# Kernel tuning notes

Hardware: AMD Instinct MI355X
Metric: run time of the kernel (lower is better)

Reference implementation:

```python
import jax, jax.numpy as jnp
import numpy as np

# Mamba-2 dims (from wrapper: d_model=hidden_size=2048, d_state=64, d_conv=4, expand=2, headdim=64)
D_MODEL = 2048
EXPAND = 2
HEADDIM = 64
D_STATE = 64
D_CONV = 4
D_INNER = EXPAND * D_MODEL            # 4096
NHEADS = D_INNER // HEADDIM           # 64
NGROUPS = 1                           # mamba_ssm default
CONV_DIM = D_INNER + 2 * NGROUPS * D_STATE          # 4224
D_IN_PROJ = 2 * D_INNER + 2 * NGROUPS * D_STATE + NHEADS  # 8384
BATCH = 1
SEQLEN = 1024
RMS_EPS = 1e-5


def setup_inputs() -> dict:
    key = jax.random.key(0)
    ks = jax.random.split(key, 8)
    x = jax.random.normal(ks[0], (BATCH, SEQLEN, D_MODEL), jnp.float32)
    W_in = jax.random.normal(ks[1], (D_IN_PROJ, D_MODEL), jnp.float32) * 0.02
    conv_w = jax.random.normal(ks[2], (CONV_DIM, D_CONV), jnp.float32) * 0.2
    conv_b = jnp.zeros((CONV_DIM,), jnp.float32)
    # dt_bias so that softplus(dt_raw + dt_bias) lands in a realistic dt range ~[1e-3, 5e-2]
    dt_bias = jax.random.uniform(ks[3], (NHEADS,), jnp.float32, -6.0, -3.0)
    # A = -exp(A_log), A_log init like mamba_ssm: A ~ Uniform(1, 16)
    A_log = jnp.log(1.0 + 15.0 * jax.random.uniform(ks[4], (NHEADS,), jnp.float32))
    D = jnp.ones((NHEADS,), jnp.float32)
    norm_w = jnp.ones((D_INNER,), jnp.float32)
    W_out = jax.random.normal(ks[5], (D_MODEL, D_INNER), jnp.float32) * 0.02
    return {"x": x, "W_in": W_in, "conv_w": conv_w, "conv_b": conv_b,
            "dt_bias": dt_bias, "A_log": A_log, "D": D, "norm_w": norm_w, "W_out": W_out}


def reference(x, W_in, conv_w, conv_b, dt_bias, A_log, D, norm_w, W_out):
    B, T, _ = x.shape
    # input projection -> [z | xBC | dt]
    zxbcdt = jnp.einsum('btd,pd->btp', x, W_in)
    z = zxbcdt[..., :D_INNER]                                  # [B,T,D_INNER] gate
    xBC = zxbcdt[..., D_INNER:D_INNER + CONV_DIM]              # [B,T,CONV_DIM]
    dt = jax.nn.softplus(zxbcdt[..., D_INNER + CONV_DIM:] + dt_bias)  # [B,T,H]
    # causal depthwise conv1d (kernel D_CONV) + SiLU
    xp = jnp.pad(xBC, ((0, 0), (D_CONV - 1, 0), (0, 0)))
    conv = conv_b + sum(xp[:, k:k + T, :] * conv_w[:, k] for k in range(D_CONV))
    xBC = jax.nn.silu(conv)
    xh = xBC[..., :D_INNER].reshape(B, T, NHEADS, HEADDIM)     # [B,T,H,P]
    Bm = xBC[..., D_INNER:D_INNER + D_STATE]                   # [B,T,N] (ngroups=1)
    Cm = xBC[..., D_INNER + D_STATE:]                          # [B,T,N]
    A = -jnp.exp(A_log)                                        # [H], negative
    dA = jnp.exp(dt * A)                                       # [B,T,H] decay per step

    def step(h, inp):
        # h: [B,H,P,N]
        dA_t, dt_t, B_t, x_t, C_t = inp
        h = h * dA_t[:, :, None, None] + jnp.einsum('bh,bn,bhp->bhpn', dt_t, B_t, x_t)
        y_t = jnp.einsum('bhpn,bn->bhp', h, C_t)
        return h, y_t

    h0 = jnp.zeros((B, NHEADS, HEADDIM, D_STATE), x.dtype)
    xs = (dA.transpose(1, 0, 2), dt.transpose(1, 0, 2), Bm.transpose(1, 0, 2),
          xh.transpose(1, 0, 2, 3), Cm.transpose(1, 0, 2))
    _, ys = jax.lax.scan(step, h0, xs)                         # ys: [T,B,H,P]
    y = ys.transpose(1, 0, 2, 3) + D[None, None, :, None] * xh  # skip term D*x
    y = y.reshape(B, T, D_INNER)
    # gated RMSNorm (norm_before_gate=False): norm(y * silu(z)) * weight
    y = y * jax.nn.silu(z)
    y = y * jax.lax.rsqrt(jnp.mean(y * y, axis=-1, keepdims=True) + RMS_EPS) * norm_w
    return jnp.einsum('bti,di->btd', y, W_out)
```

## Files before the change

### kernel.cpp

```cpp
#include <hip/hip_runtime.h>
#include <hip/hip_bf16.h>
#include <stdint.h>

#define SEQLEN   1024
#define DMODEL   2048
#define DINNER   4096
#define NHEADS   64
#define HEADDIM  64
#define DSTATE   64
#define CONVDIM  4224
#define DINPROJ  8384
#define RMS_EPS  1e-5f
#define CPAD     68
#define LP       72

typedef __attribute__((ext_vector_type(8))) __bf16 bf16x8;
typedef __attribute__((ext_vector_type(8))) unsigned short us8;
typedef __attribute__((ext_vector_type(4))) float f32x4;

__device__ __forceinline__ ushort f2bf(float f) {
    uint32_t u = __float_as_uint(f);
    u += 0x7FFFu + ((u >> 16) & 1u);
    return (ushort)(u >> 16);
}

__device__ __forceinline__ float bf2f(ushort u) {
    return __uint_as_float((uint32_t)u << 16);
}

__device__ __forceinline__ float silu(float a) { return a / (1.f + __expf(-a)); }

__device__ __forceinline__ void gload_lds16(const void* g, void* l) {
    __builtin_amdgcn_global_load_lds(
        (const __attribute__((address_space(1))) void*)g,
        (__attribute__((address_space(3))) void*)l, 16, 0, 0);
}

__global__ __launch_bounds__(256) void cvt3_kernel(
    const float* __restrict__ a, ushort* __restrict__ oa, int na4,
    const float* __restrict__ b, ushort* __restrict__ ob, int nb4,
    const float* __restrict__ c, ushort* __restrict__ oc, int nc4)
{
    int i = blockIdx.x * 256 + threadIdx.x;
    const float* src; ushort* dst;
    if (i < na4) { src = a; dst = oa; }
    else if (i < na4 + nb4) { i -= na4; src = b; dst = ob; }
    else { i -= na4 + nb4; if (i >= nc4) return; src = c; dst = oc; }
    float4 v = ((const float4*)src)[i];
    ushort4 o;
    o.x = f2bf(v.x); o.y = f2bf(v.y); o.z = f2bf(v.z); o.w = f2bf(v.w);
    ((ushort4*)dst)[i] = o;
}

__global__ __launch_bounds__(256, 4) void gemm4_bf16_nt(
    const __bf16* __restrict__ A, const __bf16* __restrict__ B,
    float* __restrict__ C, int M, int N, int K,
    int ntx, int nty, int nk, int ksteps, int swz)
{
    __shared__ __align__(16) __bf16 As[2][128 * 32];
    __shared__ __align__(16) __bf16 Bs[2][128 * 32];
    const int tid  = threadIdx.x;
    const int lane = tid & 63;
    const int wave = tid >> 6;
    const int wr = wave >> 1, wc = wave & 1;
    int id = blockIdx.x;
    if (swz) { int q = (ntx * nty * nk) >> 3; id = (id & 7) * q + (id >> 3); }
    const int kz  = id / (ntx * nty);
    const int rem = id % (ntx * nty);
    const int tx = rem / nty, ty = rem % nty;
    const int row0 = ty * 128, col0 = tx * 128;
    const int lr = lane & 15, lq = lane >> 4;
    const int rA = lane >> 2, jl = lane & 3;
    const int k0 = kz * ksteps * 32;

    const __bf16* srcA[2];
    const __bf16* srcB[2];
    int dstAB[2];
    #pragma unroll
    for (int e = 0; e < 2; ++e) {
        int r0 = (wave * 2 + e) * 16;
        int r  = r0 + rA;
        int jg = jl ^ ((rA >> 1) & 3);
        srcA[e] = A + (size_t)(row0 + r) * K + k0 + jg * 8;
        int gb = col0 + r; if (gb > N - 1) gb = N - 1;
        srcB[e] = B + (size_t)gb * K + k0 + jg * 8;
        dstAB[e] = r0 * 32;
    }

    f32x4 acc[4][4] = {};
    const int nt = ksteps;

#define STAGE(BUF)                                                            \
    _Pragma("unroll")                                                         \
    for (int e = 0; e < 2; ++e) {                                             \
        gload_lds16(srcA[e], &As[BUF][dstAB[e]]);                             \
        gload_lds16(srcB[e], &Bs[BUF][dstAB[e]]);                             \
        srcA[e] += 32; srcB[e] += 32;                                         \
    }

#define COMPUTE(BUF)                                                          \
    {                                                                         \
        bf16x8 af[4], bfr[4];                                                 \
        const int sl = (lq ^ ((lr >> 1) & 3)) * 8;                            \
        _Pragma("unroll")                                                     \
        for (int m = 0; m < 4; ++m) {                                         \
            int r = wr * 64 + m * 16 + lr;                                    \
            af[m] = *(const bf16x8*)(&As[BUF][r * 32 + sl]);                  \
        }                                                                     \
        _Pragma("unroll")                                                     \
        for (int n = 0; n < 4; ++n) {                                         \
            int r = wc * 64 + n * 16 + lr;                                    \
            bfr[n] = *(const bf16x8*)(&Bs[BUF][r * 32 + sl]);                 \
        }                                                                     \
        __builtin_amdgcn_s_setprio(1);                                        \
        _Pragma("unroll")                                                     \
        for (int m = 0; m < 4; ++m)                                           \
            _Pragma("unroll")                                                 \
            for (int n = 0; n < 4; ++n)                                       \
                acc[m][n] = __builtin_amdgcn_mfma_f32_16x16x32_bf16(af[m], bfr[n], acc[m][n], 0, 0, 0); \
        __builtin_amdgcn_s_setprio(0);                                        \
    }

    STAGE(0);
    asm volatile("s_waitcnt vmcnt(0)" ::: "memory");
    __builtin_amdgcn_s_barrier();
    asm volatile("" ::: "memory");

    for (int t = 0; t < nt; t += 2) {
        STAGE(1);
        COMPUTE(0);
        asm volatile("s_waitcnt vmcnt(0)" ::: "memory");
        __builtin_amdgcn_s_barrier();
        asm volatile("" ::: "memory");
        if (t + 2 < nt) { STAGE(0); }
        COMPUTE(1);
        asm volatile("s_waitcnt vmcnt(0)" ::: "memory");
        __builtin_amdgcn_s_barrier();
        asm volatile("" ::: "memory");
    }
#undef STAGE
#undef COMPUTE

    float* Co = C + (size_t)kz * M * N;
    #pragma unroll
    for (int m = 0; m < 4; ++m)
        #pragma unroll
        for (int n = 0; n < 4; ++n) {
            int col = col0 + wc * 64 + n * 16 + lr;
            if (col < N) {
                #pragma unroll
                for (int j = 0; j < 4; ++j) {
                    int row = row0 + wr * 64 + m * 16 + lq * 4 + j;
                    Co[(size_t)row * N + col] = acc[m][n][j];
                }
            }
        }
}

__global__ __launch_bounds__(256) void reduce4_scale_kernel(
    const float* __restrict__ p, const float* __restrict__ ssbuf,
    float* __restrict__ out, int n4)
{
    int i = blockIdx.x * 256 + threadIdx.x;
    if (i < n4) {
        int t = i >> 9;
        float sc = rsqrtf(ssbuf[t] * (1.f / DINNER) + RMS_EPS);
        float4 a = ((const float4*)p)[i];
        float4 b = ((const float4*)p)[i + n4];
        float4 c = ((const float4*)p)[i + 2 * (size_t)n4];
        float4 d = ((const float4*)p)[i + 3 * (size_t)n4];
        float4 o = {(a.x + b.x + c.x + d.x) * sc, (a.y + b.y + c.y + d.y) * sc,
                    (a.z + b.z + c.z + d.z) * sc, (a.w + b.w + c.w + d.w) * sc};
        ((float4*)out)[i] = o;
    }
}

__global__ __launch_bounds__(256, 4) void chunk_intra_kernel(
    const float* __restrict__ zx, const float* __restrict__ conv_w,
    const float* __restrict__ conv_b, const float* __restrict__ dt_bias,
    const float* __restrict__ A_log,
    float* __restrict__ x_scan, float* __restrict__ Cb,
    float* __restrict__ yintra, float* __restrict__ Tc, float* __restrict__ Ssum)
{
    const int head  = blockIdx.x >> 4;
    const int chunk = blockIdx.x & 15;
    const int t0 = chunk * 64;
    const int tid = threadIdx.x;
    const int lane = tid & 63, wv = tid >> 6;
    const int lr = lane & 15, lq = lane >> 4;

    __shared__ __align__(16) ushort XT [64 * LP];
    __shared__ __align__(16) ushort Crm[64 * LP];
    __shared__ __align__(16) ushort Brm[64 * LP];
    __shared__ __align__(16) ushort BnT[64 * LP];
    __shared__ float Sc[64], dts[64], ws[64];

    {
        const int p = lane;
        const int c = head * 64 + p;
        const float w0 = conv_w[c*4+0], w1 = conv_w[c*4+1];
        const float w2 = conv_w[c*4+2], w3 = conv_w[c*4+3];
        const float bia = conv_b[c];
        const int gt0 = t0 + wv * 16;
        const float* zc = zx + DINNER + c;
        float xm3 = (gt0 >= 3) ? zc[(size_t)(gt0-3)*DINPROJ] : 0.f;
        float xm2 = (gt0 >= 2) ? zc[(size_t)(gt0-2)*DINPROJ] : 0.f;
        float xm1 = (gt0 >= 1) ? zc[(size_t)(gt0-1)*DINPROJ] : 0.f;
        uint32_t pk[8];
        #pragma unroll
        for (int e = 0; e < 16; ++e) {
            float xt = zc[(size_t)(gt0+e)*DINPROJ];
            float s  = silu(bia + xm3*w0 + xm2*w1 + xm1*w2 + xt*w3);
            x_scan[(size_t)(gt0+e)*DINNER + c] = s;
            ushort b = f2bf(s);
            if (e & 1) pk[e>>1] |= (uint32_t)b << 16; else pk[e>>1] = (uint32_t)b;
            xm3 = xm2; xm2 = xm1; xm1 = xt;
        }
        int4 lo = { (int)pk[0], (int)pk[1], (int)pk[2], (int)pk[3] };
        int4 hi = { (int)pk[4], (int)pk[5], (int)pk[6], (int)pk[7] };
        *(int4*)&XT[p * LP + wv*16]     = lo;
        *(int4*)&XT[p * LP + wv*16 + 8] = hi;
    }

    #pragma unroll
    for (int k = 0; k < 4; ++k) {
        int n0 = wv * 16 + k * 4;
        int gt = t0 + lane;
        {
            float4 w0 = *(const float4*)&conv_w[(4096 + n0 + 0) * 4];
            float4 w1 = *(const float4*)&conv_w[(4096 + n0 + 1) * 4];
            float4 w2 = *(const float4*)&conv_w[(4096 + n0 + 2) * 4];
            float4 w3 = *(const float4*)&conv_w[(4096 + n0 + 3) * 4];
            float4 bv = *(const float4*)&conv_b[4096 + n0];
            float4 r0 = {0,0,0,0}, r1 = {0,0,0,0}, r2 = {0,0,0,0}, r3;
            const float* base = zx + (size_t)gt * DINPROJ + 8192 + n0;
            if (gt >= 3) r0 = *(const float4*)(base - 3 * DINPROJ);
            if (gt >= 2) r1 = *(const float4*)(base - 2 * DINPROJ);
            if (gt >= 1) r2 = *(const float4*)(base - 1 * DINPROJ);
            r3 = *(const float4*)base;
            ushort b0 = f2bf(silu(bv.x + r0.x*w0.x + r1.x*w0.y + r2.x*w0.z + r3.x*w0.w));
            ushort b1 = f2bf(silu(bv.y + r0.y*w1.x + r1.y*w1.y + r2.y*w1.z + r3.y*w1.w));
            ushort b2 = f2bf(silu(bv.z + r0.z*w2.x + r1.z*w2.y + r2.z*w2.z + r3.z*w2.w));
            ushort b3 = f2bf(silu(bv.w + r0.w*w3.x + r1.w*w3.y + r2.w*w3.z + r3.w*w3.w));
            uint2 pk = { (uint32_t)b0 | ((uint32_t)b1 << 16),
                         (uint32_t)b2 | ((uint32_t)b3 << 16) };
            *(uint2*)&Brm[lane * LP + n0] = pk;
            BnT[(n0+0)*LP + lane] = b0; BnT[(n0+1)*LP + lane] = b1;
            BnT[(n0+2)*LP + lane] = b2; BnT[(n0+3)*LP + lane] = b3;
        }
        {
            float4 w0 = *(const float4*)&conv_w[(4160 + n0 + 0) * 4];
            float4 w1 = *(const float4*)&conv_w[(4160 + n0 + 1) * 4];
            float4 w2 = *(const float4*)&conv_w[(4160 + n0 + 2) * 4];
            float4 w3 = *(const float4*)&conv_w[(4160 + n0 + 3) * 4];
            float4 bv = *(const float4*)&conv_b[4160 + n0];
            float4 r0 = {0,0,0,0}, r1 = {0,0,0,0}, r2 = {0,0,0,0}, r3;
            const float* base = zx + (size_t)gt * DINPROJ + 8256 + n0;
            if (gt >= 3) r0 = *(const float4*)(base - 3 * DINPROJ);
            if (gt >= 2) r1 = *(const float4*)(base - 2 * DINPROJ);
            if (gt >= 1) r2 = *(const float4*)(base - 1 * DINPROJ);
            r3 = *(const float4*)base;
            float4 cv;
            cv.x = silu(bv.x + r0.x*w0.x + r1.x*w0.y + r2.x*w0.z + r3.x*w0.w);
            cv.y = silu(bv.y + r0.y*w1.x + r1.y*w1.y + r2.y*w1.z + r3.y*w1.w);
            cv.z = silu(bv.z + r0.z*w2.x + r1.z*w2.y + r2.z*w2.z + r3.z*w2.w);
            cv.w = silu(bv.w + r0.w*w3.x + r1.w*w3.y + r2.w*w3.z + r3.w*w3.w);
            uint2 pk = { (uint32_t)f2bf(cv.x) | ((uint32_t)f2bf(cv.y) << 16),
                         (uint32_t)f2bf(cv.z) | ((uint32_t)f2bf(cv.w) << 16) };
            *(uint2*)&Crm[lane * LP + n0] = pk;
            if (head == 0) *(float4*)&Cb[(size_t)gt * 64 + n0] = cv;
        }
    }

    if (wv == 1) {
        float raw = zx[(size_t)(t0 + lane) * DINPROJ + 8320 + head] + dt_bias[head];
        float dt  = (raw > 20.f) ? raw : log1pf(__expf(raw));
        dts[lane] = dt;
        float v = dt * (-__expf(A_log[head]));
        #pragma unroll
        for (int off = 1; off < 64; off <<= 1) {
            float u = __shfl_up(v, off, 64);
            if (lane >= off) v += u;
        }
        Sc[lane] = v;
        Ssum[(t0 + lane) * 64 + head] = v;
    }
    __syncthreads();
    if (tid < 64) ws[tid] = dts[tid] * __expf(Sc[63] - Sc[tid]);

    const int i0 = wv * 16;
    f32x4 gf[4] = {};
    #pragma unroll
    for (int kk = 0; kk < 2; ++kk) {
        bf16x8 a = __builtin_bit_cast(bf16x8,
            *(const us8*)&Crm[(i0 + lr) * LP + lq*8 + kk*32]);
        #pragma unroll
        for (int f = 0; f < 4; ++f) {
            bf16x8 b = __builtin_bit_cast(bf16x8,
                *(const us8*)&Brm[(f*16 + lr) * LP + lq*8 + kk*32]);
            gf[f] = __builtin_amdgcn_mfma_f32_16x16x32_bf16(a, b, gf[f], 0, 0, 0);
        }
    }
    {
        float Si[4];
        #pragma unroll
        for (int j = 0; j < 4; ++j) Si[j] = Sc[i0 + lq*4 + j];
        #pragma unroll
        for (int f = 0; f < 4; ++f) {
            int s = f*16 + lr;
            float dw = dts[s], Ss_ = Sc[s];
            #pragma unroll
            for (int j = 0; j < 4; ++j) {
                int i = i0 + lq*4 + j;
                float v = (s <= i) ? gf[f][j] * dw * __expf(Si[j] - Ss_) : 0.f;
                Crm[i * LP + s] = f2bf(v);
            }
        }
    }
    __syncthreads();

    const int p0 = i0;
    bf16x8 xa[2], xw[2];
    #pragma unroll
    for (int kk = 0; kk < 2; ++kk) {
        us8 raw = *(const us8*)&XT[(p0 + lr) * LP + lq*8 + kk*32];
        xa[kk] = __builtin_bit_cast(bf16x8, raw);
        us8 sw;
        #pragma unroll
        for (int e = 0; e < 8; ++e) {
            int s = lq*8 + kk*32 + e;
            sw[e] = f2bf(bf2f(raw[e]) * ws[s]);
        }
        xw[kk] = __builtin_bit_cast(bf16x8, sw);
    }
    f32x4 yf[4] = {};
    f32x4 tf[4] = {};
    #pragma unroll
    for (int kk = 0; kk < 2; ++kk) {
        #pragma unroll
        for (int f = 0; f < 4; ++f) {
            bf16x8 gb = __builtin_bit_cast(bf16x8,
                *(const us8*)&Crm[(f*16 + lr) * LP + lq*8 + kk*32]);
            yf[f] = __builtin_amdgcn_mfma_f32_16x16x32_bf16(xa[kk], gb, yf[f], 0, 0, 0);
            bf16x8 bb = __builtin_bit_cast(bf16x8,
                *(const us8*)&BnT[(f*16 + lr) * LP + lq*8 + kk*32]);
            tf[f] = __builtin_amdgcn_mfma_f32_16x16x32_bf16(xw[kk], bb, tf[f], 0, 0, 0);
        }
    }
    float* tcb = Tc + (size_t)(head * 16 + chunk) * 4096;
    #pragma unroll
    for (int f = 0; f < 4; ++f) {
        int col = f*16 + lr;
        int p   = p0 + lq*4;
        float4 yv = {yf[f][0], yf[f][1], yf[f][2], yf[f][3]};
        *(float4*)&yintra[(size_t)(t0 + col) * DINNER + head*64 + p] = yv;
        #pragma unroll
        for (int j = 0; j < 4; ++j)
            tcb[(p + j) * 64 + col] = tf[f][j];
    }
}

__global__ __launch_bounds__(256) void chunk_state_kernel(
    float* __restrict__ Tc, const float* __restrict__ Ssum)
{
    const int head = blockIdx.x;
    const int tid = threadIdx.x;
    float h[16] = {};
    float* base = Tc + (size_t)head * 16 * 4096 + tid * 16;
    for (int c = 0; c < 16; ++c) {
        float Q = __expf(Ssum[(c * 64 + 63) * 64 + head]);
        float4* p = (float4*)(base + (size_t)c * 4096);
        #pragma unroll
        for (int v = 0; v < 4; ++v) {
            float4 t = p[v];
            float4 hold = {h[v*4], h[v*4+1], h[v*4+2], h[v*4+3]};
            h[v*4+0] = h[v*4+0] * Q + t.x;
            h[v*4+1] = h[v*4+1] * Q + t.y;
            h[v*4+2] = h[v*4+2] * Q + t.z;
            h[v*4+3] = h[v*4+3] * Q + t.w;
            p[v] = hold;
        }
    }
}

__global__ __launch_bounds__(256) void inter_combine_kernel(
    const float* __restrict__ Hpre, const float* __restrict__ Cb,
    const float* __restrict__ Ssum, const float* __restrict__ yintra,
    const float* __restrict__ x_scan, const float* __restrict__ zx,
    const float* __restrict__ Dv, const float* __restrict__ norm_w,
    ushort* __restrict__ ybf, float* __restrict__ ssbuf)
{
    const int head  = blockIdx.x >> 4;
    const int chunk = blockIdx.x & 15;
    const int t0 = chunk * 64;
    const int tid = threadIdx.x;
    const int ty = tid >> 4, tx = tid & 15;
    const int lane = tid & 63, wv = tid >> 6;

    __shared__ __align__(16) float HsT[64][CPAD];
    __shared__ __align__(16) float CsT[64][CPAD];
    __shared__ float Se[64];

    const float* hb = Hpre + (size_t)(head * 16 + chunk) * 4096;
    #pragma unroll
    for (int k = 0; k < 4; ++k) {
        int n0 = wv * 16 + k * 4;
        float4 h = *(const float4*)&hb[lane * 64 + n0];
        float4 c = *(const float4*)&Cb[(t0 + lane) * 64 + n0];
        HsT[n0][lane] = h.x; HsT[n0+1][lane] = h.y; HsT[n0+2][lane] = h.z; HsT[n0+3][lane] = h.w;
        CsT[n0][lane] = c.x; CsT[n0+1][lane] = c.y; CsT[n0+2][lane] = c.z; CsT[n0+3][lane] = c.w;
    }
    if (tid < 64) Se[tid] = __expf(Ssum[(t0 + tid) * 64 + head]);
    __syncthreads();

    float acc[4][4] = {};
    for (int n = 0; n < 64; ++n) {
        float4 ci = *(const float4*)&CsT[n][ty * 4];
        float4 hp = *(const float4*)&HsT[n][tx * 4];
        acc[0][0] += ci.x*hp.x; acc[0][1] += ci.x*hp.y; acc[0][2] += ci.x*hp.z; acc[0][3] += ci.x*hp.w;
        acc[1][0] += ci.y*hp.x; acc[1][1] += ci.y*hp.y; acc[1][2] += ci.y*hp.z; acc[1][3] += ci.y*hp.w;
        acc[2][0] += ci.z*hp.x; acc[2][1] += ci.z*hp.y; acc[2][2] += ci.z*hp.z; acc[2][3] += ci.z*hp.w;
        acc[3][0] += ci.w*hp.x; acc[3][1] += ci.w*hp.y; acc[3][2] += ci.w*hp.z; acc[3][3] += ci.w*hp.w;
    }

    const float Dh = Dv[head];
    const int col = head * 64 + tx * 4;
    float4 nw = *(const float4*)&norm_w[col];
    float ssp[4];
    #pragma unroll
    for (int di = 0; di < 4; ++di) {
        int t = t0 + ty * 4 + di;
        float se = Se[ty * 4 + di];
        float4 yi = *(const float4*)&yintra[(size_t)t * DINNER + col];
        float4 xh = *(const float4*)&x_scan[(size_t)t * DINNER + col];
        float4 zv = *(const float4*)&zx[(size_t)t * DINPROJ + col];
        float4 y;
        y.x = (acc[di][0] * se + yi.x + Dh * xh.x) * silu(zv.x);
        y.y = (acc[di][1] * se + yi.y + Dh * xh.y) * silu(zv.y);
        y.z = (acc[di][2] * se + yi.z + Dh * xh.z) * silu(zv.z);
        y.w = (acc[di][3] * se + yi.w + Dh * xh.w) * silu(zv.w);
        ssp[di] = y.x*y.x + y.y*y.y + y.z*y.z + y.w*y.w;
        ushort4 o;
        o.x = f2bf(y.x * nw.x); o.y = f2bf(y.y * nw.y);
        o.z = f2bf(y.z * nw.z); o.w = f2bf(y.w * nw.w);
        *(ushort4*)&ybf[(size_t)t * DINNER + col] = o;
    }
    #pragma unroll
    for (int di = 0; di < 4; ++di) {
        float s = ssp[di];
        s += __shfl_xor(s, 1, 64);
        s += __shfl_xor(s, 2, 64);
        s += __shfl_xor(s, 4, 64);
        s += __shfl_xor(s, 8, 64);
        if (tx == 0) atomicAdd(&ssbuf[t0 + ty * 4 + di], s);
    }
}

extern "C" void kernel_launch(void* const* d_in, const int* in_sizes, int n_in,
                              void* d_out, int out_size, void* d_ws, size_t ws_size,
                              hipStream_t stream)
{
    const float* x       = (const float*)d_in[0];
    const float* W_in    = (const float*)d_in[1];
    const float* conv_w  = (const float*)d_in[2];
    const float* conv_b  = (const float*)d_in[3];
    const float* dt_bias = (const float*)d_in[4];
    const float* A_log   = (const float*)d_in[5];
    const float* Dv      = (const float*)d_in[6];
    const float* norm_w  = (const float*)d_in[7];
    const float* W_out   = (const float*)d_in[8];
    float* out = (float*)d_out;

    char* ws = (char*)d_ws;
    const size_t OFF_WIN  = 0;
    const size_t OFF_WOUT = 34340864;
    const size_t OFF_XBF  = OFF_WOUT + 16777216;
    const size_t OFF_ZX   = OFF_XBF + 4194304;
    const size_t OFF_XSC  = OFF_ZX + 34340864;
    const size_t OFF_CB   = OFF_XSC + 16777216;
    const size_t OFF_SSB  = OFF_CB + 262144;
    const size_t OFF_YBF  = OFF_SSB + 4096;
    const size_t OFF_TC   = OFF_YBF + 8388608;
    const size_t OFF_SS   = OFF_TC + 16777216;

    ushort* WinBf  = (ushort*)(ws + OFF_WIN);
    ushort* WoutBf = (ushort*)(ws + OFF_WOUT);
    ushort* xBf    = (ushort*)(ws + OFF_XBF);
    float*  zxb    = (float*)(ws + OFF_ZX);
    float*  xsc    = (float*)(ws + OFF_XSC);
    float*  Cb     = (float*)(ws + OFF_CB);
    float*  ssbuf  = (float*)(ws + OFF_SSB);
    ushort* ybf    = (ushort*)(ws + OFF_YBF);
    float*  Tc     = (float*)(ws + OFF_TC);
    float*  Ssum   = (float*)(ws + OFF_SS);
    float*  yintra = (float*)(ws + OFF_WIN);
    float*  part   = (float*)(ws + OFF_WIN);

    const int nW4 = DINPROJ * DMODEL / 4;
    const int nO4 = DMODEL * DINNER / 4;
    const int nX4 = SEQLEN * DMODEL / 4;
    const int nAll = nW4 + nO4 + nX4;
    cvt3_kernel<<<(nAll + 255) / 256, 256, 0, stream>>>(
        W_in, WinBf, nW4, W_out, WoutBf, nO4, x, xBf, nX4);

    hipMemsetAsync(ssbuf, 0, SEQLEN * sizeof(float), stream);

    gemm4_bf16_nt<<<528, 256, 0, stream>>>(
        (const __bf16*)xBf, (const __bf16*)WinBf, zxb,
        SEQLEN, DINPROJ, DMODEL, 66, 8, 1, DMODEL / 32, 1);

    chunk_intra_kernel<<<1024, 256, 0, stream>>>(
        zxb, conv_w, conv_b, dt_bias, A_log, xsc, Cb, yintra, Tc, Ssum);

    chunk_state_kernel<<<64, 256, 0, stream>>>(Tc, Ssum);

    inter_combine_kernel<<<1024, 256, 0, stream>>>(
        Tc, Cb, Ssum, yintra, xsc, zxb, Dv, norm_w, ybf, ssbuf);

    gemm4_bf16_nt<<<512, 256, 0, stream>>>(
        (const __bf16*)ybf, (const __bf16*)WoutBf, part,
        SEQLEN, DMODEL, DINNER, 16, 8, 4, DINNER / 32 / 4, 1);

    reduce4_scale_kernel<<<(SEQLEN * DMODEL / 4 + 255) / 256, 256, 0, stream>>>(
        part, ssbuf, out, SEQLEN * DMODEL / 4);
}
```

Baseline: 185.2 us.

## Halve GEMM M-tile to 64 rows and fold ssbuf zeroing into convert kernel

The bf16 GEMM tile shrinks from 128x128 to 64x128, so each wave computes 2x4 MFMA tiles instead of 4x4 and loads one A row-chunk per stage. Both projection launches double their grid size (1056 and 1024 blocks) to raise the block count on the device's CUs. The separate hipMemsetAsync of the RMS sum-of-squares buffer is removed, and block 0 of the convert kernel zeroes it instead, saving one stream operation. The smaller tile lowers reuse per block, adding operand traffic and LDS loads per MFMA, in exchange for better occupancy and load balance.

```diff
diff --git a/kernel.cpp b/kernel.cpp
--- a/kernel.cpp
+++ b/kernel.cpp
@@ -39,9 +39,14 @@
 __global__ __launch_bounds__(256) void cvt3_kernel(
     const float* __restrict__ a, ushort* __restrict__ oa, int na4,
     const float* __restrict__ b, ushort* __restrict__ ob, int nb4,
-    const float* __restrict__ c, ushort* __restrict__ oc, int nc4)
+    const float* __restrict__ c, ushort* __restrict__ oc, int nc4,
+    float* __restrict__ ssbuf)
 {
     int i = blockIdx.x * 256 + threadIdx.x;
+    if (blockIdx.x == 0) {
+        float4 z = {0.f, 0.f, 0.f, 0.f};
+        ((float4*)ssbuf)[threadIdx.x] = z;
+    }
     const float* src; ushort* dst;
     if (i < na4) { src = a; dst = oa; }
     else if (i < na4 + nb4) { i -= na4; src = b; dst = ob; }
@@ -57,7 +62,7 @@
     float* __restrict__ C, int M, int N, int K,
     int ntx, int nty, int nk, int ksteps, int swz)
 {
-    __shared__ __align__(16) __bf16 As[2][128 * 32];
+    __shared__ __align__(16) __bf16 As[2][64 * 32];
     __shared__ __align__(16) __bf16 Bs[2][128 * 32];
     const int tid  = threadIdx.x;
     const int lane = tid & 63;
@@ -68,43 +73,52 @@
     const int kz  = id / (ntx * nty);
     const int rem = id % (ntx * nty);
     const int tx = rem / nty, ty = rem % nty;
-    const int row0 = ty * 128, col0 = tx * 128;
+    const int row0 = ty * 64, col0 = tx * 128;
     const int lr = lane & 15, lq = lane >> 4;
     const int rA = lane >> 2, jl = lane & 3;
     const int k0 = kz * ksteps * 32;
 
-    const __bf16* srcA[2];
+    const __bf16* srcA;
     const __bf16* srcB[2];
-    int dstAB[2];
+    int dstA, dstB[2];
+    {
+        int r0 = wave * 16;
+        int r  = r0 + rA;
+        int jg = jl ^ ((rA >> 1) & 3);
+        srcA = A + (size_t)(row0 + r) * K + k0 + jg * 8;
+        dstA = r0 * 32;
+    }
     #pragma unroll
     for (int e = 0; e < 2; ++e) {
         int r0 = (wave * 2 + e) * 16;
         int r  = r0 + rA;
         int jg = jl ^ ((rA >> 1) & 3);
-        srcA[e] = A + (size_t)(row0 + r) * K + k0 + jg * 8;
         int gb = col0 + r; if (gb > N - 1) gb = N - 1;
         srcB[e] = B + (size_t)gb * K + k0 + jg * 8;
-        dstAB[e] = r0 * 32;
-    }
-
-    f32x4 acc[4][4] = {};
+        dstB[e] = r0 * 32;
+    }
+
+    f32x4 acc[2][4] = {};
     const int nt = ksteps;
 
 #define STAGE(BUF)                                                            \
-    _Pragma("unroll")                                                         \
-    for (int e = 0; e < 2; ++e) {                                             \
-        gload_lds16(srcA[e], &As[BUF][dstAB[e]]);                             \
-        gload_lds16(srcB[e], &Bs[BUF][dstAB[e]]);                             \
-        srcA[e] += 32; srcB[e] += 32;                                         \
+    {                                                                         \
+        gload_lds16(srcA, &As[BUF][dstA]);                                    \
+        srcA += 32;                                                           \
+        _Pragma("unroll")                                                     \
+        for (int e = 0; e < 2; ++e) {                                         \
+            gload_lds16(srcB[e], &Bs[BUF][dstB[e]]);                          \
+            srcB[e] += 32;                                                    \
+        }                                                                     \
     }
 
 #define COMPUTE(BUF)                                                          \
     {                                                                         \
-        bf16x8 af[4], bfr[4];                                                 \
+        bf16x8 af[2], bfr[4];                                                 \
         const int sl = (lq ^ ((lr >> 1) & 3)) * 8;                            \
         _Pragma("unroll")                                                     \
-        for (int m = 0; m < 4; ++m) {                                         \
-            int r = wr * 64 + m * 16 + lr;                                    \
+        for (int m = 0; m < 2; ++m) {                                         \
+            int r = wr * 32 + m * 16 + lr;                                    \
             af[m] = *(const bf16x8*)(&As[BUF][r * 32 + sl]);                  \
         }                                                                     \
         _Pragma("unroll")                                                     \
@@ -114,7 +128,7 @@
         }                                                                     \
         __builtin_amdgcn_s_setprio(1);                                        \
         _Pragma("unroll")                                                     \
-        for (int m = 0; m < 4; ++m)                                           \
+        for (int m = 0; m < 2; ++m)                                           \
             _Pragma("unroll")                                                 \
             for (int n = 0; n < 4; ++n)                                       \
                 acc[m][n] = __builtin_amdgcn_mfma_f32_16x16x32_bf16(af[m], bfr[n], acc[m][n], 0, 0, 0); \
@@ -143,14 +157,14 @@
 
     float* Co = C + (size_t)kz * M * N;
     #pragma unroll
-    for (int m = 0; m < 4; ++m)
+    for (int m = 0; m < 2; ++m)
         #pragma unroll
         for (int n = 0; n < 4; ++n) {
             int col = col0 + wc * 64 + n * 16 + lr;
             if (col < N) {
                 #pragma unroll
                 for (int j = 0; j < 4; ++j) {
-                    int row = row0 + wr * 64 + m * 16 + lq * 4 + j;
+                    int row = row0 + wr * 32 + m * 16 + lq * 4 + j;
                     Co[(size_t)row * N + col] = acc[m][n][j];
                 }
             }
@@ -501,13 +515,11 @@
     const int nX4 = SEQLEN * DMODEL / 4;
     const int nAll = nW4 + nO4 + nX4;
     cvt3_kernel<<<(nAll + 255) / 256, 256, 0, stream>>>(
-        W_in, WinBf, nW4, W_out, WoutBf, nO4, x, xBf, nX4);
-
-    hipMemsetAsync(ssbuf, 0, SEQLEN * sizeof(float), stream);
-
-    gemm4_bf16_nt<<<528, 256, 0, stream>>>(
+        W_in, WinBf, nW4, W_out, WoutBf, nO4, x, xBf, nX4, ssbuf);
+
+    gemm4_bf16_nt<<<1056, 256, 0, stream>>>(
         (const __bf16*)xBf, (const __bf16*)WinBf, zxb,
-        SEQLEN, DINPROJ, DMODEL, 66, 8, 1, DMODEL / 32, 1);
+        SEQLEN, DINPROJ, DMODEL, 66, 16, 1, DMODEL / 32, 1);
 
     chunk_intra_kernel<<<1024, 256, 0, stream>>>(
         zxb, conv_w, conv_b, dt_bias, A_log, xsc, Cb, yintra, Tc, Ssum);
@@ -517,9 +529,9 @@
     inter_combine_kernel<<<1024, 256, 0, stream>>>(
         Tc, Cb, Ssum, yintra, xsc, zxb, Dv, norm_w, ybf, ssbuf);
 
-    gemm4_bf16_nt<<<512, 256, 0, stream>>>(
+    gemm4_bf16_nt<<<1024, 256, 0, stream>>>(
         (const __bf16*)ybf, (const __bf16*)WoutBf, part,
-        SEQLEN, DMODEL, DINNER, 16, 8, 4, DINNER / 32 / 4, 1);
+        SEQLEN, DMODEL, DINNER, 16, 16, 4, DINNER / 32 / 4, 1);
 
     reduce4_scale_kernel<<<(SEQLEN * DMODEL / 4 + 255) / 256, 256, 0, stream>>>(
         part, ssbuf, out, SEQLEN * DMODEL / 4);
```

After: 195.9 us. 5.8% more time.

## Overlap W_out bf16 conversion with input-projection GEMM and fold memset into convert

Applied to the files above, without the earlier changes.

The W_out fp32-to-bf16 conversion moves out of the upfront convert kernel and into 160 extra blocks appended to the first GEMM launch, so it runs alongside the GEMM tiles. The ssbuf zeroing is folded into the first block of the convert kernel, which removes a separate memset launch. This shortens the serial convert phase and drops one launch, at the cost of the extra blocks competing with GEMM tiles for CU slots and memory bandwidth.

```diff
diff --git a/kernel.cpp b/kernel.cpp
--- a/kernel.cpp
+++ b/kernel.cpp
@@ -36,16 +36,19 @@
         (__attribute__((address_space(3))) void*)l, 16, 0, 0);
 }
 
-__global__ __launch_bounds__(256) void cvt3_kernel(
+__global__ __launch_bounds__(256) void cvt2_kernel(
     const float* __restrict__ a, ushort* __restrict__ oa, int na4,
-    const float* __restrict__ b, ushort* __restrict__ ob, int nb4,
-    const float* __restrict__ c, ushort* __restrict__ oc, int nc4)
+    const float* __restrict__ c, ushort* __restrict__ oc, int nc4,
+    float* __restrict__ ssbuf)
 {
     int i = blockIdx.x * 256 + threadIdx.x;
+    if (blockIdx.x == 0) {
+        float4 z = {0.f, 0.f, 0.f, 0.f};
+        ((float4*)ssbuf)[threadIdx.x] = z;
+    }
     const float* src; ushort* dst;
     if (i < na4) { src = a; dst = oa; }
-    else if (i < na4 + nb4) { i -= na4; src = b; dst = ob; }
-    else { i -= na4 + nb4; if (i >= nc4) return; src = c; dst = oc; }
+    else { i -= na4; if (i >= nc4) return; src = c; dst = oc; }
     float4 v = ((const float4*)src)[i];
     ushort4 o;
     o.x = f2bf(v.x); o.y = f2bf(v.y); o.z = f2bf(v.z); o.w = f2bf(v.w);
@@ -55,10 +58,22 @@
 __global__ __launch_bounds__(256, 4) void gemm4_bf16_nt(
     const __bf16* __restrict__ A, const __bf16* __restrict__ B,
     float* __restrict__ C, int M, int N, int K,
-    int ntx, int nty, int nk, int ksteps, int swz)
+    int ntx, int nty, int nk, int ksteps, int swz, int ngemm,
+    const float* __restrict__ cvt_src, ushort* __restrict__ cvt_dst, int cvt_n4)
 {
     __shared__ __align__(16) __bf16 As[2][128 * 32];
     __shared__ __align__(16) __bf16 Bs[2][128 * 32];
+    if (blockIdx.x >= ngemm) {
+        int nblk = gridDim.x - ngemm;
+        for (int i = (blockIdx.x - ngemm) * 256 + threadIdx.x; i < cvt_n4;
+             i += nblk * 256) {
+            float4 v = ((const float4*)cvt_src)[i];
+            ushort4 o;
+            o.x = f2bf(v.x); o.y = f2bf(v.y); o.z = f2bf(v.z); o.w = f2bf(v.w);
+            ((ushort4*)cvt_dst)[i] = o;
+        }
+        return;
+    }
     const int tid  = threadIdx.x;
     const int lane = tid & 63;
     const int wave = tid >> 6;
@@ -499,15 +514,13 @@
     const int nW4 = DINPROJ * DMODEL / 4;
     const int nO4 = DMODEL * DINNER / 4;
     const int nX4 = SEQLEN * DMODEL / 4;
-    const int nAll = nW4 + nO4 + nX4;
-    cvt3_kernel<<<(nAll + 255) / 256, 256, 0, stream>>>(
-        W_in, WinBf, nW4, W_out, WoutBf, nO4, x, xBf, nX4);
-
-    hipMemsetAsync(ssbuf, 0, SEQLEN * sizeof(float), stream);
-
-    gemm4_bf16_nt<<<528, 256, 0, stream>>>(
+    cvt2_kernel<<<(nW4 + nX4 + 255) / 256, 256, 0, stream>>>(
+        W_in, WinBf, nW4, x, xBf, nX4, ssbuf);
+
+    gemm4_bf16_nt<<<528 + 160, 256, 0, stream>>>(
         (const __bf16*)xBf, (const __bf16*)WinBf, zxb,
-        SEQLEN, DINPROJ, DMODEL, 66, 8, 1, DMODEL / 32, 1);
+        SEQLEN, DINPROJ, DMODEL, 66, 8, 1, DMODEL / 32, 1, 528,
+        W_out, WoutBf, nO4);
 
     chunk_intra_kernel<<<1024, 256, 0, stream>>>(
         zxb, conv_w, conv_b, dt_bias, A_log, xsc, Cb, yintra, Tc, Ssum);
@@ -519,7 +532,8 @@
 
     gemm4_bf16_nt<<<512, 256, 0, stream>>>(
         (const __bf16*)ybf, (const __bf16*)WoutBf, part,
-        SEQLEN, DMODEL, DINNER, 16, 8, 4, DINNER / 32 / 4, 1);
+        SEQLEN, DMODEL, DINNER, 16, 8, 4, DINNER / 32 / 4, 1, 512,
+        nullptr, nullptr, 0);
 
     reduce4_scale_kernel<<<(SEQLEN * DMODEL / 4 + 255) / 256, 256, 0, stream>>>(
         part, ssbuf, out, SEQLEN * DMODEL / 4);
```

New measurement: 176.4 us, median of 2. -4.8%, faster.
